# Kernel optimization log

Hardware: AMD Instinct MI355X
Metric: run time of the kernel (lower is better)

The kernel has to match this reference:

```python
import jax, jax.numpy as jnp
import numpy as np

D_MODEL = 1024
NUM_HEADS = 16

def setup_inputs() -> dict:
    key = jax.random.key(0)
    ks = jax.random.split(key, 5)
    std = np.sqrt(2.0 / (D_MODEL + D_MODEL))
    def w(k):
        # trunc_normal approx: normal clipped to +-3 std
        v = jax.random.truncated_normal(k, -3.0, 3.0, (D_MODEL, D_MODEL), dtype=jnp.float32) * std
        return v
    return {
        "x": jax.random.normal(ks[0], (2, 2048, D_MODEL), dtype=jnp.float32),
        "w_q": w(ks[1]),
        "w_k": w(ks[2]),
        "w_v": w(ks[3]),
        "w_o": w(ks[4]),
    }

def reference(x, w_q, w_k, w_v, w_o):
    B, S, D = x.shape
    H = NUM_HEADS
    dk = D // H
    # Linear: y = x @ W^T  (weight is [d_out, d_in])
    def proj(w):
        y = jnp.einsum('bsd,ed->bse', x, w)
        return y.reshape(B, S, H, dk).transpose(0, 2, 1, 3)  # [B,H,S,dk]
    q, k, v = proj(w_q), proj(w_k), proj(w_v)
    scale = 1.0 / jnp.sqrt(jnp.float32(dk))
    scores = jnp.einsum('bhqd,bhkd->bhqk', q, k) * scale  # [B,H,S,S]
    causal = jnp.tril(jnp.ones((S, S), dtype=bool))
    scores = jnp.where(causal, scores, -jnp.inf)
    attn = jax.nn.softmax(scores, axis=-1)
    out = jnp.einsum('bhqk,bhkd->bhqd', attn, v)  # [B,H,S,dk]
    out = out.transpose(0, 2, 1, 3).reshape(B, S, D)
    return jnp.einsum('bsd,ed->bse', out, w_o)
```

## Files before the change

### kernel.cpp

```cpp
#include <hip/hip_runtime.h>
#include <hip/hip_bf16.h>
#include <stdint.h>

#define S_LEN 2048
#define DM    1024
#define NH    16
#define DK    64
#define NBATCH 2

typedef __attribute__((ext_vector_type(8))) short bf8_t;
typedef __attribute__((ext_vector_type(4))) short s4_t;
typedef __attribute__((ext_vector_type(4))) float f4_t;

using bf16 = __hip_bfloat16;

#define NEG_BIG (-1.0e30f)
#define SCALE2  (0.125f * 1.44269504088896f)

static __device__ __forceinline__ f4_t mfma16(bf8_t a, bf8_t b, f4_t c) {
    return __builtin_amdgcn_mfma_f32_16x16x32_bf16(a, b, c, 0, 0, 0);
}

static __device__ __forceinline__ short f2b(float f) {
    __hip_bfloat16 h = __float2bfloat16(f);
    return *reinterpret_cast<short*>(&h);
}

static __device__ __forceinline__ void g2l16(const bf16* g, bf16* l) {
#if __has_builtin(__builtin_amdgcn_global_load_lds)
    __builtin_amdgcn_global_load_lds(
        (const __attribute__((address_space(1))) void*)g,
        (__attribute__((address_space(3))) void*)l, 16, 0, 0);
#else
    *(bf8_t*)l = *(const bf8_t*)g;
#endif
}

__global__ __launch_bounds__(256)
void cvt_all(const float* __restrict__ x,  const float* __restrict__ wq,
             const float* __restrict__ wk, const float* __restrict__ wv,
             const float* __restrict__ wo, bf16* __restrict__ ob) {
    const size_t SEG = 1u << 20;
    size_t i = ((size_t)blockIdx.x * 256 + threadIdx.x) * 8;
    const float* src;
    if      (i < 4 * SEG) src = x  + i;
    else if (i < 5 * SEG) src = wq + (i - 4 * SEG);
    else if (i < 6 * SEG) src = wk + (i - 5 * SEG);
    else if (i < 7 * SEG) src = wv + (i - 6 * SEG);
    else                  src = wo + (i - 7 * SEG);
    float4 f0 = *(const float4*)(src);
    float4 f1 = *(const float4*)(src + 4);
    bf8_t v;
    v[0]=f2b(f0.x); v[1]=f2b(f0.y); v[2]=f2b(f0.z); v[3]=f2b(f0.w);
    v[4]=f2b(f1.x); v[5]=f2b(f1.y); v[6]=f2b(f1.z); v[7]=f2b(f1.w);
    *(bf8_t*)(ob + i) = v;
}

#define GEMM_B_MAINLOOP(Aptr, Bptr)                                          \
    __shared__ bf16 As[128][32];                                             \
    __shared__ bf16 Bs[128][32];                                             \
    const int tid  = threadIdx.x;                                            \
    const int lane = tid & 63;                                               \
    const int w    = tid >> 6;                                               \
    const int wr   = w >> 1, wc = w & 1;                                     \
    const int lhi  = lane >> 4, llo = lane & 15;                             \
    const int bm   = blockIdx.x * 128;                                       \
    const int bn   = blockIdx.y * 128;                                       \
    const int r0c  = tid >> 2;                           \
    const int c0c  = (tid & 3) << 3;                     \
    const int r1c  = (256 + tid) >> 2;                                       \
    f4_t acc[4][4] = {};                                                     \
    for (int k0 = 0; k0 < 1024; k0 += 32) {                                  \
        __syncthreads();                                                     \
        g2l16(Aptr + (size_t)(bm + r0c) * 1024 + k0 + c0c,                   \
              &As[0][0] + (size_t)tid * 8);                                  \
        g2l16(Aptr + (size_t)(bm + r1c) * 1024 + k0 + c0c,                   \
              &As[0][0] + (size_t)(256 + tid) * 8);                          \
        g2l16(Bptr + (size_t)(bn + r0c) * 1024 + k0 + c0c,                   \
              &Bs[0][0] + (size_t)tid * 8);                                  \
        g2l16(Bptr + (size_t)(bn + r1c) * 1024 + k0 + c0c,                   \
              &Bs[0][0] + (size_t)(256 + tid) * 8);                          \
        asm volatile("s_waitcnt vmcnt(0)" ::: "memory");                     \
        __syncthreads();                                                     \
        bf8_t af[4], bfr[4];                                                 \
        _Pragma("unroll")                                                    \
        for (int i = 0; i < 4; ++i) {                                        \
            af[i]  = *(const bf8_t*)(&As[wr * 64 + i * 16 + llo][lhi * 8]);  \
            bfr[i] = *(const bf8_t*)(&Bs[wc * 64 + i * 16 + llo][lhi * 8]);  \
        }                                                                    \
        _Pragma("unroll")                                                    \
        for (int mi = 0; mi < 4; ++mi)                                       \
            _Pragma("unroll")                                                \
            for (int ni = 0; ni < 4; ++ni)                                   \
                acc[mi][ni] = mfma16(af[mi], bfr[ni], acc[mi][ni]);          \
    }

__global__ __launch_bounds__(256)
void gemm_qkv_b(const bf16* __restrict__ xb,
                const bf16* __restrict__ wqb, const bf16* __restrict__ wkb,
                const bf16* __restrict__ wvb,
                bf16* __restrict__ qws, bf16* __restrict__ kws,
                bf16* __restrict__ vtws) {
    const int z = blockIdx.z;
    const bf16* Wb = (z == 0) ? wqb : (z == 1) ? wkb : wvb;
    GEMM_B_MAINLOOP(xb, Wb)

    if (z < 2) {
        bf16* C = z ? kws : qws;
        const float sc = z ? 1.0f : SCALE2;
        #pragma unroll
        for (int mi = 0; mi < 4; ++mi)
            #pragma unroll
            for (int ni = 0; ni < 4; ++ni)
                #pragma unroll
                for (int r = 0; r < 4; ++r) {
                    int m = bm + wr * 64 + mi * 16 + lhi * 4 + r;
                    int n = bn + wc * 64 + ni * 16 + llo;
                    int b = m >> 11, s = m & (S_LEN - 1);
                    int h = n >> 6,  d = n & (DK - 1);
                    C[(((size_t)(b * NH + h) * S_LEN) + s) * DK + d] =
                        __float2bfloat16(acc[mi][ni][r] * sc);
                }
    } else {
        #pragma unroll
        for (int mi = 0; mi < 4; ++mi)
            #pragma unroll
            for (int ni = 0; ni < 4; ++ni) {
                int m0 = bm + wr * 64 + mi * 16 + lhi * 4;
                int n  = bn + wc * 64 + ni * 16 + llo;
                int b = m0 >> 11, s0 = m0 & (S_LEN - 1);
                int h = n >> 6,   d  = n & (DK - 1);
                s4_t pk;
                #pragma unroll
                for (int r = 0; r < 4; ++r) pk[r] = f2b(acc[mi][ni][r]);
                *(s4_t*)&vtws[(((size_t)(b * NH + h) * DK) + d) * S_LEN + s0] = pk;
            }
    }
}

__global__ __launch_bounds__(256)
void gemm_o_b(const bf16* __restrict__ A, const bf16* __restrict__ Wb,
              float* __restrict__ C) {
    __shared__ bf16 As[128][32];
    __shared__ bf16 Bs[64][32];
    const int tid  = threadIdx.x;
    const int lane = tid & 63;
    const int w    = tid >> 6;
    const int wr   = w >> 1, wc = w & 1;
    const int lhi  = lane >> 4, llo = lane & 15;
    const int bm   = blockIdx.x * 128;
    const int bn   = blockIdx.y * 64;
    const int r0c  = tid >> 2;
    const int c0c  = (tid & 3) << 3;
    const int r1c  = (256 + tid) >> 2;
    f4_t acc[4][2] = {};
    for (int k0 = 0; k0 < 1024; k0 += 32) {
        __syncthreads();
        g2l16(A + (size_t)(bm + r0c) * 1024 + k0 + c0c,
              &As[0][0] + (size_t)tid * 8);
        g2l16(A + (size_t)(bm + r1c) * 1024 + k0 + c0c,
              &As[0][0] + (size_t)(256 + tid) * 8);
        g2l16(Wb + (size_t)(bn + r0c) * 1024 + k0 + c0c,
              &Bs[0][0] + (size_t)tid * 8);
        asm volatile("s_waitcnt vmcnt(0)" ::: "memory");
        __syncthreads();
        bf8_t af[4], bfr[2];
        #pragma unroll
        for (int i = 0; i < 4; ++i)
            af[i] = *(const bf8_t*)(&As[wr * 64 + i * 16 + llo][lhi * 8]);
        #pragma unroll
        for (int i = 0; i < 2; ++i)
            bfr[i] = *(const bf8_t*)(&Bs[wc * 32 + i * 16 + llo][lhi * 8]);
        #pragma unroll
        for (int mi = 0; mi < 4; ++mi)
            #pragma unroll
            for (int ni = 0; ni < 2; ++ni)
                acc[mi][ni] = mfma16(af[mi], bfr[ni], acc[mi][ni]);
    }
    #pragma unroll
    for (int mi = 0; mi < 4; ++mi)
        #pragma unroll
        for (int ni = 0; ni < 2; ++ni)
            #pragma unroll
            for (int r = 0; r < 4; ++r) {
                int m = bm + wr * 64 + mi * 16 + lhi * 4 + r;
                int n = bn + wc * 32 + ni * 16 + llo;
                C[(size_t)m * DM + n] = acc[mi][ni][r];
            }
}

__global__ __launch_bounds__(256)
void gemm_qkv_f32(const float* __restrict__ x,
                  const float* __restrict__ wqp, const float* __restrict__ wkp,
                  const float* __restrict__ wvp,
                  bf16* __restrict__ qws, bf16* __restrict__ kws,
                  bf16* __restrict__ vtws) {
    constexpr int K = DM;
    constexpr int BM = 128, BK = 32, LDT = BK + 8;
    const int z = blockIdx.z;
    const float* W = (z == 0) ? wqp : (z == 1) ? wkp : wvp;
    __shared__ bf16 As[BM][LDT];
    __shared__ bf16 Bs[BM][LDT];
    const int tid  = threadIdx.x;
    const int lane = tid & 63;
    const int w    = tid >> 6;
    const int wr   = w >> 1, wc = w & 1;
    const int lhi  = lane >> 4, llo = lane & 15;
    const int bm   = blockIdx.x * BM;
    const int bn   = blockIdx.y * BM;
    f4_t acc[4][4] = {};
    for (int k0 = 0; k0 < K; k0 += BK) {
        __syncthreads();
        #pragma unroll
        for (int t = 0; t < 2; ++t) {
            int c   = t * 256 + tid;
            int row = c >> 2;
            int col = (c & 3) << 3;
            {
                const float* s0 = x + (size_t)(bm + row) * K + k0 + col;
                float4 f0 = *(const float4*)(s0);
                float4 f1 = *(const float4*)(s0 + 4);
                bf8_t a8;
                a8[0]=f2b(f0.x); a8[1]=f2b(f0.y); a8[2]=f2b(f0.z); a8[3]=f2b(f0.w);
                a8[4]=f2b(f1.x); a8[5]=f2b(f1.y); a8[6]=f2b(f1.z); a8[7]=f2b(f1.w);
                *(bf8_t*)(&As[row][col]) = a8;
            }
            {
                const float* s0 = W + (size_t)(bn + row) * K + k0 + col;
                float4 f0 = *(const float4*)(s0);
                float4 f1 = *(const float4*)(s0 + 4);
                bf8_t b8;
                b8[0]=f2b(f0.x); b8[1]=f2b(f0.y); b8[2]=f2b(f0.z); b8[3]=f2b(f0.w);
                b8[4]=f2b(f1.x); b8[5]=f2b(f1.y); b8[6]=f2b(f1.z); b8[7]=f2b(f1.w);
                *(bf8_t*)(&Bs[row][col]) = b8;
            }
        }
        __syncthreads();
        bf8_t af[4], bfr[4];
        #pragma unroll
        for (int i = 0; i < 4; ++i) {
            af[i]  = *(const bf8_t*)(&As[wr * 64 + i * 16 + llo][lhi * 8]);
            bfr[i] = *(const bf8_t*)(&Bs[wc * 64 + i * 16 + llo][lhi * 8]);
        }
        #pragma unroll
        for (int mi = 0; mi < 4; ++mi)
            #pragma unroll
            for (int ni = 0; ni < 4; ++ni)
                acc[mi][ni] = mfma16(af[mi], bfr[ni], acc[mi][ni]);
    }
    if (z < 2) {
        bf16* C = z ? kws : qws;
        const float sc = z ? 1.0f : SCALE2;
        #pragma unroll
        for (int mi = 0; mi < 4; ++mi)
            #pragma unroll
            for (int ni = 0; ni < 4; ++ni)
                #pragma unroll
                for (int r = 0; r < 4; ++r) {
                    int m = bm + wr * 64 + mi * 16 + lhi * 4 + r;
                    int n = bn + wc * 64 + ni * 16 + llo;
                    int b = m >> 11, s = m & (S_LEN - 1);
                    int h = n >> 6,  d = n & (DK - 1);
                    C[(((size_t)(b * NH + h) * S_LEN) + s) * DK + d] =
                        __float2bfloat16(acc[mi][ni][r] * sc);
                }
    } else {
        #pragma unroll
        for (int mi = 0; mi < 4; ++mi)
            #pragma unroll
            for (int ni = 0; ni < 4; ++ni) {
                int m0 = bm + wr * 64 + mi * 16 + lhi * 4;
                int n  = bn + wc * 64 + ni * 16 + llo;
                int b = m0 >> 11, s0 = m0 & (S_LEN - 1);
                int h = n >> 6,   d  = n & (DK - 1);
                s4_t pk;
                #pragma unroll
                for (int r = 0; r < 4; ++r) pk[r] = f2b(acc[mi][ni][r]);
                *(s4_t*)&vtws[(((size_t)(b * NH + h) * DK) + d) * S_LEN + s0] = pk;
            }
    }
}

__global__ __launch_bounds__(256)
void gemm_o_f32(const bf16* __restrict__ A, const float* __restrict__ W,
                float* __restrict__ C) {
    constexpr int N = DM;
    constexpr int K = DM;
    constexpr int BM = 128, BN = 64, BK = 32, LDT = BK + 8;
    __shared__ bf16 As[BM][LDT];
    __shared__ bf16 Bs[BN][LDT];
    const int tid  = threadIdx.x;
    const int lane = tid & 63;
    const int w    = tid >> 6;
    const int wr   = w >> 1, wc = w & 1;
    const int lhi  = lane >> 4, llo = lane & 15;
    const int bm   = blockIdx.x * BM;
    const int bn   = blockIdx.y * BN;
    f4_t acc[4][2] = {};
    for (int k0 = 0; k0 < K; k0 += BK) {
        __syncthreads();
        #pragma unroll
        for (int t = 0; t < 2; ++t) {
            int c   = t * 256 + tid;
            int row = c >> 2;
            int col = (c & 3) << 3;
            *(bf8_t*)(&As[row][col]) =
                *(const bf8_t*)(A + (size_t)(bm + row) * K + k0 + col);
        }
        {
            int row = tid >> 2;
            int col = (tid & 3) << 3;
            const float* s0 = W + (size_t)(bn + row) * K + k0 + col;
            float4 f0 = *(const float4*)(s0);
            float4 f1 = *(const float4*)(s0 + 4);
            bf8_t b8;
            b8[0]=f2b(f0.x); b8[1]=f2b(f0.y); b8[2]=f2b(f0.z); b8[3]=f2b(f0.w);
            b8[4]=f2b(f1.x); b8[5]=f2b(f1.y); b8[6]=f2b(f1.z); b8[7]=f2b(f1.w);
            *(bf8_t*)(&Bs[row][col]) = b8;
        }
        __syncthreads();
        bf8_t af[4], bfr[2];
        #pragma unroll
        for (int i = 0; i < 4; ++i)
            af[i] = *(const bf8_t*)(&As[wr * 64 + i * 16 + llo][lhi * 8]);
        #pragma unroll
        for (int i = 0; i < 2; ++i)
            bfr[i] = *(const bf8_t*)(&Bs[wc * 32 + i * 16 + llo][lhi * 8]);
        #pragma unroll
        for (int mi = 0; mi < 4; ++mi)
            #pragma unroll
            for (int ni = 0; ni < 2; ++ni)
                acc[mi][ni] = mfma16(af[mi], bfr[ni], acc[mi][ni]);
    }
    #pragma unroll
    for (int mi = 0; mi < 4; ++mi)
        #pragma unroll
        for (int ni = 0; ni < 2; ++ni)
            #pragma unroll
            for (int r = 0; r < 4; ++r) {
                int m = bm + wr * 64 + mi * 16 + lhi * 4 + r;
                int n = bn + wc * 32 + ni * 16 + llo;
                C[(size_t)m * N + n] = acc[mi][ni][r];
            }
}

__global__ __launch_bounds__(512, 4)
void attn_fwd(const bf16* __restrict__ Q, const bf16* __restrict__ K,
              const bf16* __restrict__ Vt, bf16* __restrict__ AO) {
    __shared__ bf16 Ks[2][64][64];
    __shared__ bf16 Vs[2][64][64];

    const int bh = blockIdx.x;
    const int qt = 15 - (int)blockIdx.y;
    const int q0 = qt * 128;
    const int nt = 2 * qt + 2;

    const bf16* Qh = Q  + (size_t)bh * S_LEN * DK;
    const bf16* Kh = K  + (size_t)bh * S_LEN * DK;
    const bf16* Vh = Vt + (size_t)bh * DK * S_LEN;

    const int tid  = threadIdx.x;
    const int lane = tid & 63;
    const int w    = tid >> 6;
    const int lhi  = lane >> 4, llo = lane & 15;
    const int qw   = q0 + w * 16;
    const int sw   = llo & 7;

    const int srow = tid >> 3;
    const int schk = (tid & 7) ^ (srow & 7);
    const int gk = (((srow >> 2) & 3) << 3) | (((srow >> 4) & 1) << 2)
                 | (srow & 3) | ((srow >> 5) << 5);

#define STAGE(kv, b)                                                          \
    do {                                                                      \
        g2l16(Kh + (size_t)((kv) + gk) * DK + schk * 8,                       \
              &Ks[b][0][0] + (size_t)tid * 8);                                \
        g2l16(Vh + (size_t)srow * S_LEN + (kv) + schk * 8,                    \
              &Vs[b][0][0] + (size_t)tid * 8);                                \
    } while (0)

    const bf16* qrow = Qh + (size_t)(q0 + w * 16 + llo) * DK;
    const bf8_t qf0 = *(const bf8_t*)(qrow + lhi * 8);
    const bf8_t qf1 = *(const bf8_t*)(qrow + 32 + lhi * 8);

    bf8_t ones;
    #pragma unroll
    for (int j = 0; j < 8; ++j) ones[j] = (short)0x3F80;

    STAGE(0, 0);
    asm volatile("s_waitcnt vmcnt(0)" ::: "memory");
    __syncthreads();

    f4_t o[4] = {};
    float lr[4] = {0.f, 0.f, 0.f, 0.f};
    float mr = NEG_BIG;

    for (int t = 0; t < nt; ++t) {
        const int kv0 = t * 64;
        const int cur = t & 1;

        if (t + 1 < nt) STAGE((t + 1) * 64, cur ^ 1);

        if (kv0 <= qw + 15) {
            f4_t s[4] = {};
            __builtin_amdgcn_s_setprio(1);
            #pragma unroll
            for (int nf = 0; nf < 4; ++nf) {
                const int R = nf * 16 + llo;
                bf8_t k0f = *(const bf8_t*)&Ks[cur][R][(lhi ^ sw) * 8];
                bf8_t k1f = *(const bf8_t*)&Ks[cur][R][((4 + lhi) ^ sw) * 8];
                s[nf] = mfma16(k0f, qf0, s[nf]);
                s[nf] = mfma16(k1f, qf1, s[nf]);
            }
            __builtin_amdgcn_s_setprio(0);

            if (kv0 + 63 > qw) {
                #pragma unroll
                for (int nf = 0; nf < 4; ++nf)
                    #pragma unroll
                    for (int r = 0; r < 4; ++r)
                        if (kv0 + lhi * 8 + ((nf & 1) << 2) + r + ((nf >> 1) << 5)
                            > qw + llo)
                            s[nf][r] = NEG_BIG;
            }

            float pm = s[0][0];
            #pragma unroll
            for (int nf = 0; nf < 4; ++nf)
                #pragma unroll
                for (int r = 0; r < 4; ++r) pm = fmaxf(pm, s[nf][r]);
            pm = fmaxf(pm, __shfl_xor(pm, 16));
            pm = fmaxf(pm, __shfl_xor(pm, 32));

            if (__any(pm > mr + 8.0f)) {
                float mn = fmaxf(mr, pm);
                float alpha = exp2f(mr - mn);
                mr = mn;
                float ao[4];
                #pragma unroll
                for (int r = 0; r < 4; ++r) ao[r] = __shfl(alpha, lhi * 4 + r);
                #pragma unroll
                for (int df = 0; df < 4; ++df)
                    #pragma unroll
                    for (int r = 0; r < 4; ++r) o[df][r] *= ao[r];
                #pragma unroll
                for (int r = 0; r < 4; ++r) lr[r] *= ao[r];
            }

            bf8_t pa0, pa1;
            #pragma unroll
            for (int r = 0; r < 4; ++r) {
                pa0[r]     = f2b(exp2f(s[0][r] - mr));
                pa0[4 + r] = f2b(exp2f(s[1][r] - mr));
                pa1[r]     = f2b(exp2f(s[2][r] - mr));
                pa1[4 + r] = f2b(exp2f(s[3][r] - mr));
            }

            f4_t rsacc = {};
            rsacc = mfma16(pa0, ones, rsacc);
            rsacc = mfma16(pa1, ones, rsacc);

            __builtin_amdgcn_s_setprio(1);
            #pragma unroll
            for (int df = 0; df < 4; ++df) {
                const int R = df * 16 + llo;
                bf8_t vb0 = *(const bf8_t*)&Vs[cur][R][(lhi ^ sw) * 8];
                bf8_t vb1 = *(const bf8_t*)&Vs[cur][R][((4 + lhi) ^ sw) * 8];
                o[df] = mfma16(pa0, vb0, o[df]);
                o[df] = mfma16(pa1, vb1, o[df]);
            }
            __builtin_amdgcn_s_setprio(0);

            #pragma unroll
            for (int r = 0; r < 4; ++r) lr[r] += rsacc[r];
        }

        asm volatile("s_waitcnt vmcnt(0)" ::: "memory");
        __syncthreads();
    }
#undef STAGE

    const int b = bh >> 4, h = bh & (NH - 1);
    #pragma unroll
    for (int r = 0; r < 4; ++r) {
        float inv = 1.0f / lr[r];
        int q = q0 + w * 16 + lhi * 4 + r;
        bf16* orow = AO + ((size_t)(b * S_LEN + q) * DM) + h * DK;
        #pragma unroll
        for (int df = 0; df < 4; ++df)
            orow[df * 16 + llo] = __float2bfloat16(o[df][r] * inv);
    }
}

extern "C" void kernel_launch(void* const* d_in, const int* in_sizes, int n_in,
                              void* d_out, int out_size, void* d_ws, size_t ws_size,
                              hipStream_t stream) {
    const float* x  = (const float*)d_in[0];
    const float* wq = (const float*)d_in[1];
    const float* wk = (const float*)d_in[2];
    const float* wv = (const float*)d_in[3];
    const float* wo = (const float*)d_in[4];
    float* out = (float*)d_out;

    const size_t SEG   = 1u << 20;
    const size_t elems = 4 * SEG;
    const size_t need_fast = (8 * SEG + 3 * elems) * sizeof(bf16);

    dim3 blk(256);

    if (ws_size >= need_fast) {
        bf16* ob   = (bf16*)d_ws;
        bf16* xb   = ob;
        bf16* wqb  = ob + 4 * SEG;
        bf16* wkb  = ob + 5 * SEG;
        bf16* wvb  = ob + 6 * SEG;
        bf16* wob  = ob + 7 * SEG;
        bf16* qws  = ob + 8 * SEG;
        bf16* kws  = qws + elems;
        bf16* vtws = kws + elems;
        bf16* aws  = xb;

        cvt_all<<<4096, blk, 0, stream>>>(x, wq, wk, wv, wo, ob);
        gemm_qkv_b<<<dim3(32, 8, 3), blk, 0, stream>>>(xb, wqb, wkb, wvb,
                                                       qws, kws, vtws);
        attn_fwd<<<dim3(NBATCH * NH, 16), dim3(512), 0, stream>>>(qws, kws, vtws, aws);
        gemm_o_b<<<dim3(32, 16), blk, 0, stream>>>(aws, wob, out);
    } else {
        if (ws_size < elems * 4 * sizeof(bf16)) return;
        bf16* qws  = (bf16*)d_ws;
        bf16* kws  = qws + elems;
        bf16* vtws = kws + elems;
        bf16* aws  = vtws + elems;

        gemm_qkv_f32<<<dim3(32, 8, 3), blk, 0, stream>>>(x, wq, wk, wv,
                                                         qws, kws, vtws);
        attn_fwd<<<dim3(NBATCH * NH, 16), dim3(512), 0, stream>>>(qws, kws, vtws, aws);
        gemm_o_f32<<<dim3(32, 16), blk, 0, stream>>>(aws, wo, out);
    }
}
```

Baseline: 113.4 us.

## Process two 16-row query tiles per wave in attention with 256-thread blocks

The attention kernel drops from 512 to 256 threads per block, and each wave now handles two 16-row query tiles (A and B) instead of one. Each K and V fragment read from LDS feeds twice as many MFMAs, and each thread stages twice as many global-to-LDS chunks. This roughly halves LDS read traffic per unit of work and the number of waves sharing a barrier. The cost is higher register pressure (launch bounds now 256,2) and less parallelism per block to hide latency. Causal skipping for the lower tile is handled per tile with a doA flag.

```diff
diff --git a/kernel.cpp b/kernel.cpp
--- a/kernel.cpp
+++ b/kernel.cpp
@@ -344,7 +344,7 @@
             }
 }
 
-__global__ __launch_bounds__(512, 4)
+__global__ __launch_bounds__(256, 2)
 void attn_fwd(const bf16* __restrict__ Q, const bf16* __restrict__ K,
               const bf16* __restrict__ Vt, bf16* __restrict__ AO) {
     __shared__ bf16 Ks[2][64][64];
@@ -363,25 +363,32 @@
     const int lane = tid & 63;
     const int w    = tid >> 6;
     const int lhi  = lane >> 4, llo = lane & 15;
-    const int qw   = q0 + w * 16;
+    const int qwA  = q0 + w * 32;
+    const int qwB  = qwA + 16;
     const int sw   = llo & 7;
 
-    const int srow = tid >> 3;
-    const int schk = (tid & 7) ^ (srow & 7);
-    const int gk = (((srow >> 2) & 3) << 3) | (((srow >> 4) & 1) << 2)
-                 | (srow & 3) | ((srow >> 5) << 5);
+    const int r0   = tid >> 3;
+    const int schk = (tid & 7) ^ (r0 & 7);
+    const int gk0  = (((r0 >> 2) & 3) << 3) | (((r0 >> 4) & 1) << 2) | (r0 & 3);
 
 #define STAGE(kv, b)                                                          \
     do {                                                                      \
-        g2l16(Kh + (size_t)((kv) + gk) * DK + schk * 8,                       \
+        g2l16(Kh + (size_t)((kv) + gk0) * DK + schk * 8,                      \
               &Ks[b][0][0] + (size_t)tid * 8);                                \
-        g2l16(Vh + (size_t)srow * S_LEN + (kv) + schk * 8,                    \
+        g2l16(Kh + (size_t)((kv) + gk0 + 32) * DK + schk * 8,                 \
+              &Ks[b][32][0] + (size_t)tid * 8);                               \
+        g2l16(Vh + (size_t)r0 * S_LEN + (kv) + schk * 8,                      \
               &Vs[b][0][0] + (size_t)tid * 8);                                \
+        g2l16(Vh + (size_t)(r0 + 32) * S_LEN + (kv) + schk * 8,               \
+              &Vs[b][32][0] + (size_t)tid * 8);                               \
     } while (0)
 
-    const bf16* qrow = Qh + (size_t)(q0 + w * 16 + llo) * DK;
-    const bf8_t qf0 = *(const bf8_t*)(qrow + lhi * 8);
-    const bf8_t qf1 = *(const bf8_t*)(qrow + 32 + lhi * 8);
+    const bf16* qrowA = Qh + (size_t)(qwA + llo) * DK;
+    const bf16* qrowB = Qh + (size_t)(qwB + llo) * DK;
+    const bf8_t qfA0 = *(const bf8_t*)(qrowA + lhi * 8);
+    const bf8_t qfA1 = *(const bf8_t*)(qrowA + 32 + lhi * 8);
+    const bf8_t qfB0 = *(const bf8_t*)(qrowB + lhi * 8);
+    const bf8_t qfB1 = *(const bf8_t*)(qrowB + 32 + lhi * 8);
 
     bf8_t ones;
     #pragma unroll
@@ -391,9 +398,9 @@
     asm volatile("s_waitcnt vmcnt(0)" ::: "memory");
     __syncthreads();
 
-    f4_t o[4] = {};
-    float lr[4] = {0.f, 0.f, 0.f, 0.f};
-    float mr = NEG_BIG;
+    f4_t oA[4] = {}, oB[4] = {};
+    float lrA[4] = {0.f,0.f,0.f,0.f}, lrB[4] = {0.f,0.f,0.f,0.f};
+    float mrA = NEG_BIG, mrB = NEG_BIG;
 
     for (int t = 0; t < nt; ++t) {
         const int kv0 = t * 64;
@@ -401,64 +408,108 @@
 
         if (t + 1 < nt) STAGE((t + 1) * 64, cur ^ 1);
 
-        if (kv0 <= qw + 15) {
-            f4_t s[4] = {};
+        if (kv0 <= qwB + 15) {
+            const bool doA = (kv0 <= qwA + 15);
+
+            f4_t sA[4] = {}, sB[4] = {};
             __builtin_amdgcn_s_setprio(1);
             #pragma unroll
             for (int nf = 0; nf < 4; ++nf) {
                 const int R = nf * 16 + llo;
                 bf8_t k0f = *(const bf8_t*)&Ks[cur][R][(lhi ^ sw) * 8];
                 bf8_t k1f = *(const bf8_t*)&Ks[cur][R][((4 + lhi) ^ sw) * 8];
-                s[nf] = mfma16(k0f, qf0, s[nf]);
-                s[nf] = mfma16(k1f, qf1, s[nf]);
+                sB[nf] = mfma16(k0f, qfB0, sB[nf]);
+                sB[nf] = mfma16(k1f, qfB1, sB[nf]);
+                if (doA) {
+                    sA[nf] = mfma16(k0f, qfA0, sA[nf]);
+                    sA[nf] = mfma16(k1f, qfA1, sA[nf]);
+                }
             }
             __builtin_amdgcn_s_setprio(0);
 
-            if (kv0 + 63 > qw) {
+            if (kv0 + 63 > qwB) {
                 #pragma unroll
                 for (int nf = 0; nf < 4; ++nf)
                     #pragma unroll
                     for (int r = 0; r < 4; ++r)
                         if (kv0 + lhi * 8 + ((nf & 1) << 2) + r + ((nf >> 1) << 5)
-                            > qw + llo)
-                            s[nf][r] = NEG_BIG;
-            }
-
-            float pm = s[0][0];
+                            > qwB + llo)
+                            sB[nf][r] = NEG_BIG;
+            }
+            if (doA && kv0 + 63 > qwA) {
+                #pragma unroll
+                for (int nf = 0; nf < 4; ++nf)
+                    #pragma unroll
+                    for (int r = 0; r < 4; ++r)
+                        if (kv0 + lhi * 8 + ((nf & 1) << 2) + r + ((nf >> 1) << 5)
+                            > qwA + llo)
+                            sA[nf][r] = NEG_BIG;
+            }
+
+            float pmA = NEG_BIG, pmB = sB[0][0];
             #pragma unroll
             for (int nf = 0; nf < 4; ++nf)
                 #pragma unroll
-                for (int r = 0; r < 4; ++r) pm = fmaxf(pm, s[nf][r]);
-            pm = fmaxf(pm, __shfl_xor(pm, 16));
-            pm = fmaxf(pm, __shfl_xor(pm, 32));
-
-            if (__any(pm > mr + 8.0f)) {
-                float mn = fmaxf(mr, pm);
-                float alpha = exp2f(mr - mn);
-                mr = mn;
-                float ao[4];
-                #pragma unroll
-                for (int r = 0; r < 4; ++r) ao[r] = __shfl(alpha, lhi * 4 + r);
+                for (int r = 0; r < 4; ++r) pmB = fmaxf(pmB, sB[nf][r]);
+            if (doA) {
+                pmA = sA[0][0];
+                #pragma unroll
+                for (int nf = 0; nf < 4; ++nf)
+                    #pragma unroll
+                    for (int r = 0; r < 4; ++r) pmA = fmaxf(pmA, sA[nf][r]);
+            }
+            pmB = fmaxf(pmB, __shfl_xor(pmB, 16));
+            pmB = fmaxf(pmB, __shfl_xor(pmB, 32));
+            pmA = fmaxf(pmA, __shfl_xor(pmA, 16));
+            pmA = fmaxf(pmA, __shfl_xor(pmA, 32));
+
+            if (__any(fmaxf(pmA - mrA, pmB - mrB) > 8.0f)) {
+                float mnA = fmaxf(mrA, pmA), mnB = fmaxf(mrB, pmB);
+                float aA = exp2f(mrA - mnA), aB = exp2f(mrB - mnB);
+                mrA = mnA; mrB = mnB;
+                float aoA[4], aoB[4];
+                #pragma unroll
+                for (int r = 0; r < 4; ++r) {
+                    aoA[r] = __shfl(aA, lhi * 4 + r);
+                    aoB[r] = __shfl(aB, lhi * 4 + r);
+                }
                 #pragma unroll
                 for (int df = 0; df < 4; ++df)
                     #pragma unroll
-                    for (int r = 0; r < 4; ++r) o[df][r] *= ao[r];
-                #pragma unroll
-                for (int r = 0; r < 4; ++r) lr[r] *= ao[r];
-            }
-
-            bf8_t pa0, pa1;
+                    for (int r = 0; r < 4; ++r) {
+                        oA[df][r] *= aoA[r];
+                        oB[df][r] *= aoB[r];
+                    }
+                #pragma unroll
+                for (int r = 0; r < 4; ++r) { lrA[r] *= aoA[r]; lrB[r] *= aoB[r]; }
+            }
+
+            bf8_t paA0 = ones, paA1 = ones, paB0, paB1;
             #pragma unroll
             for (int r = 0; r < 4; ++r) {
-                pa0[r]     = f2b(exp2f(s[0][r] - mr));
-                pa0[4 + r] = f2b(exp2f(s[1][r] - mr));
-                pa1[r]     = f2b(exp2f(s[2][r] - mr));
-                pa1[4 + r] = f2b(exp2f(s[3][r] - mr));
-            }
-
-            f4_t rsacc = {};
-            rsacc = mfma16(pa0, ones, rsacc);
-            rsacc = mfma16(pa1, ones, rsacc);
+                paB0[r]     = f2b(exp2f(sB[0][r] - mrB));
+                paB0[4 + r] = f2b(exp2f(sB[1][r] - mrB));
+                paB1[r]     = f2b(exp2f(sB[2][r] - mrB));
+                paB1[4 + r] = f2b(exp2f(sB[3][r] - mrB));
+            }
+            if (doA) {
+                #pragma unroll
+                for (int r = 0; r < 4; ++r) {
+                    paA0[r]     = f2b(exp2f(sA[0][r] - mrA));
+                    paA0[4 + r] = f2b(exp2f(sA[1][r] - mrA));
+                    paA1[r]     = f2b(exp2f(sA[2][r] - mrA));
+                    paA1[4 + r] = f2b(exp2f(sA[3][r] - mrA));
+                }
+            }
+
+            f4_t rsB = {};
+            rsB = mfma16(paB0, ones, rsB);
+            rsB = mfma16(paB1, ones, rsB);
+            f4_t rsA = {};
+            if (doA) {
+                rsA = mfma16(paA0, ones, rsA);
+                rsA = mfma16(paA1, ones, rsA);
+            }
 
             __builtin_amdgcn_s_setprio(1);
             #pragma unroll
@@ -466,13 +517,20 @@
                 const int R = df * 16 + llo;
                 bf8_t vb0 = *(const bf8_t*)&Vs[cur][R][(lhi ^ sw) * 8];
                 bf8_t vb1 = *(const bf8_t*)&Vs[cur][R][((4 + lhi) ^ sw) * 8];
-                o[df] = mfma16(pa0, vb0, o[df]);
-                o[df] = mfma16(pa1, vb1, o[df]);
+                oB[df] = mfma16(paB0, vb0, oB[df]);
+                oB[df] = mfma16(paB1, vb1, oB[df]);
+                if (doA) {
+                    oA[df] = mfma16(paA0, vb0, oA[df]);
+                    oA[df] = mfma16(paA1, vb1, oA[df]);
+                }
             }
             __builtin_amdgcn_s_setprio(0);
 
             #pragma unroll
-            for (int r = 0; r < 4; ++r) lr[r] += rsacc[r];
+            for (int r = 0; r < 4; ++r) {
+                lrB[r] += rsB[r];
+                if (doA) lrA[r] += rsA[r];
+            }
         }
 
         asm volatile("s_waitcnt vmcnt(0)" ::: "memory");
@@ -483,12 +541,17 @@
     const int b = bh >> 4, h = bh & (NH - 1);
     #pragma unroll
     for (int r = 0; r < 4; ++r) {
-        float inv = 1.0f / lr[r];
-        int q = q0 + w * 16 + lhi * 4 + r;
-        bf16* orow = AO + ((size_t)(b * S_LEN + q) * DM) + h * DK;
-        #pragma unroll
-        for (int df = 0; df < 4; ++df)
-            orow[df * 16 + llo] = __float2bfloat16(o[df][r] * inv);
+        float invA = 1.0f / lrA[r];
+        float invB = 1.0f / lrB[r];
+        int qA = qwA + lhi * 4 + r;
+        int qB = qwB + lhi * 4 + r;
+        bf16* orowA = AO + ((size_t)(b * S_LEN + qA) * DM) + h * DK;
+        bf16* orowB = AO + ((size_t)(b * S_LEN + qB) * DM) + h * DK;
+        #pragma unroll
+        for (int df = 0; df < 4; ++df) {
+            orowA[df * 16 + llo] = __float2bfloat16(oA[df][r] * invA);
+            orowB[df * 16 + llo] = __float2bfloat16(oB[df][r] * invB);
+        }
     }
 }
 
@@ -523,7 +586,7 @@
         cvt_all<<<4096, blk, 0, stream>>>(x, wq, wk, wv, wo, ob);
         gemm_qkv_b<<<dim3(32, 8, 3), blk, 0, stream>>>(xb, wqb, wkb, wvb,
                                                        qws, kws, vtws);
-        attn_fwd<<<dim3(NBATCH * NH, 16), dim3(512), 0, stream>>>(qws, kws, vtws, aws);
+        attn_fwd<<<dim3(NBATCH * NH, 16), blk, 0, stream>>>(qws, kws, vtws, aws);
         gemm_o_b<<<dim3(32, 16), blk, 0, stream>>>(aws, wob, out);
     } else {
         if (ws_size < elems * 4 * sizeof(bf16)) return;
@@ -534,7 +597,7 @@
 
         gemm_qkv_f32<<<dim3(32, 8, 3), blk, 0, stream>>>(x, wq, wk, wv,
                                                          qws, kws, vtws);
-        attn_fwd<<<dim3(NBATCH * NH, 16), dim3(512), 0, stream>>>(qws, kws, vtws, aws);
+        attn_fwd<<<dim3(NBATCH * NH, 16), blk, 0, stream>>>(qws, kws, vtws, aws);
         gemm_o_f32<<<dim3(32, 16), blk, 0, stream>>>(aws, wo, out);
     }
 }
```

After: 130.9 us. 15.4% more time.

## Split KV range across two warp groups per 64-row query tile with merge

Applied to the files above, without the earlier changes.

The attention kernel now processes 64 query rows per block instead of 128, and splits the KV tiles between two groups of four waves that work on alternating tiles at the same time. Each group keeps its own double-buffered K/V shared-memory tiles. At the end the partial outputs, row sums and maxima are exchanged through shared memory and merged flash-decoding style. This doubles the grid and halves the serial KV loop per wave to improve parallelism and load balance, at the cost of more redundant K/V loads, twice the shared memory, and a final merge step.

```diff
diff --git a/kernel.cpp b/kernel.cpp
--- a/kernel.cpp
+++ b/kernel.cpp
@@ -347,13 +347,14 @@
 __global__ __launch_bounds__(512, 4)
 void attn_fwd(const bf16* __restrict__ Q, const bf16* __restrict__ K,
               const bf16* __restrict__ Vt, bf16* __restrict__ AO) {
-    __shared__ bf16 Ks[2][64][64];
-    __shared__ bf16 Vs[2][64][64];
+    __shared__ bf16 Ks[2][2][64][64];
+    __shared__ bf16 Vs[2][2][64][64];
 
     const int bh = blockIdx.x;
-    const int qt = 15 - (int)blockIdx.y;
-    const int q0 = qt * 128;
-    const int nt = 2 * qt + 2;
+    const int qt = 31 - (int)blockIdx.y;
+    const int q0 = qt * 64;
+    const int nt = qt + 1;
+    const int S  = (nt + 1) >> 1;
 
     const bf16* Qh = Q  + (size_t)bh * S_LEN * DK;
     const bf16* Kh = K  + (size_t)bh * S_LEN * DK;
@@ -362,8 +363,10 @@
     const int tid  = threadIdx.x;
     const int lane = tid & 63;
     const int w    = tid >> 6;
+    const int g    = w >> 2;
+    const int qsub = w & 3;
     const int lhi  = lane >> 4, llo = lane & 15;
-    const int qw   = q0 + w * 16;
+    const int qw   = q0 + qsub * 16;
     const int sw   = llo & 7;
 
     const int srow = tid >> 3;
@@ -371,15 +374,16 @@
     const int gk = (((srow >> 2) & 3) << 3) | (((srow >> 4) & 1) << 2)
                  | (srow & 3) | ((srow >> 5) << 5);
 
-#define STAGE(kv, b)                                                          \
+#define STAGE(t, gg, b)                                                       \
     do {                                                                      \
-        g2l16(Kh + (size_t)((kv) + gk) * DK + schk * 8,                       \
-              &Ks[b][0][0] + (size_t)tid * 8);                                \
-        g2l16(Vh + (size_t)srow * S_LEN + (kv) + schk * 8,                    \
-              &Vs[b][0][0] + (size_t)tid * 8);                                \
+        const int kv_ = (t) * 64;                                             \
+        g2l16(Kh + (size_t)(kv_ + gk) * DK + schk * 8,                        \
+              &Ks[gg][b][0][0] + (size_t)tid * 8);                            \
+        g2l16(Vh + (size_t)srow * S_LEN + kv_ + schk * 8,                     \
+              &Vs[gg][b][0][0] + (size_t)tid * 8);                            \
     } while (0)
 
-    const bf16* qrow = Qh + (size_t)(q0 + w * 16 + llo) * DK;
+    const bf16* qrow = Qh + (size_t)(qw + llo) * DK;
     const bf8_t qf0 = *(const bf8_t*)(qrow + lhi * 8);
     const bf8_t qf1 = *(const bf8_t*)(qrow + 32 + lhi * 8);
 
@@ -387,7 +391,8 @@
     #pragma unroll
     for (int j = 0; j < 8; ++j) ones[j] = (short)0x3F80;
 
-    STAGE(0, 0);
+    STAGE(0, 0, 0);
+    if (1 < nt) STAGE(1, 1, 0);
     asm volatile("s_waitcnt vmcnt(0)" ::: "memory");
     __syncthreads();
 
@@ -395,22 +400,24 @@
     float lr[4] = {0.f, 0.f, 0.f, 0.f};
     float mr = NEG_BIG;
 
-    for (int t = 0; t < nt; ++t) {
-        const int kv0 = t * 64;
-        const int cur = t & 1;
-
-        if (t + 1 < nt) STAGE((t + 1) * 64, cur ^ 1);
-
-        if (kv0 <= qw + 15) {
-            f4_t s[4] = {};
+    for (int s = 0; s < S; ++s) {
+        const int tg  = 2 * s + g;
+        const int cur = s & 1;
+        const int tn0 = 2 * (s + 1);
+        if (tn0 < nt)     STAGE(tn0,     0, cur ^ 1);
+        if (tn0 + 1 < nt) STAGE(tn0 + 1, 1, cur ^ 1);
+
+        const int kv0 = tg * 64;
+        if (tg < nt && kv0 <= qw + 15) {
+            f4_t sc[4] = {};
             __builtin_amdgcn_s_setprio(1);
             #pragma unroll
             for (int nf = 0; nf < 4; ++nf) {
                 const int R = nf * 16 + llo;
-                bf8_t k0f = *(const bf8_t*)&Ks[cur][R][(lhi ^ sw) * 8];
-                bf8_t k1f = *(const bf8_t*)&Ks[cur][R][((4 + lhi) ^ sw) * 8];
-                s[nf] = mfma16(k0f, qf0, s[nf]);
-                s[nf] = mfma16(k1f, qf1, s[nf]);
+                bf8_t k0f = *(const bf8_t*)&Ks[g][cur][R][(lhi ^ sw) * 8];
+                bf8_t k1f = *(const bf8_t*)&Ks[g][cur][R][((4 + lhi) ^ sw) * 8];
+                sc[nf] = mfma16(k0f, qf0, sc[nf]);
+                sc[nf] = mfma16(k1f, qf1, sc[nf]);
             }
             __builtin_amdgcn_s_setprio(0);
 
@@ -421,14 +428,14 @@
                     for (int r = 0; r < 4; ++r)
                         if (kv0 + lhi * 8 + ((nf & 1) << 2) + r + ((nf >> 1) << 5)
                             > qw + llo)
-                            s[nf][r] = NEG_BIG;
-            }
-
-            float pm = s[0][0];
+                            sc[nf][r] = NEG_BIG;
+            }
+
+            float pm = sc[0][0];
             #pragma unroll
             for (int nf = 0; nf < 4; ++nf)
                 #pragma unroll
-                for (int r = 0; r < 4; ++r) pm = fmaxf(pm, s[nf][r]);
+                for (int r = 0; r < 4; ++r) pm = fmaxf(pm, sc[nf][r]);
             pm = fmaxf(pm, __shfl_xor(pm, 16));
             pm = fmaxf(pm, __shfl_xor(pm, 32));
 
@@ -450,10 +457,10 @@
             bf8_t pa0, pa1;
             #pragma unroll
             for (int r = 0; r < 4; ++r) {
-                pa0[r]     = f2b(exp2f(s[0][r] - mr));
-                pa0[4 + r] = f2b(exp2f(s[1][r] - mr));
-                pa1[r]     = f2b(exp2f(s[2][r] - mr));
-                pa1[4 + r] = f2b(exp2f(s[3][r] - mr));
+                pa0[r]     = f2b(exp2f(sc[0][r] - mr));
+                pa0[4 + r] = f2b(exp2f(sc[1][r] - mr));
+                pa1[r]     = f2b(exp2f(sc[2][r] - mr));
+                pa1[4 + r] = f2b(exp2f(sc[3][r] - mr));
             }
 
             f4_t rsacc = {};
@@ -464,8 +471,8 @@
             #pragma unroll
             for (int df = 0; df < 4; ++df) {
                 const int R = df * 16 + llo;
-                bf8_t vb0 = *(const bf8_t*)&Vs[cur][R][(lhi ^ sw) * 8];
-                bf8_t vb1 = *(const bf8_t*)&Vs[cur][R][((4 + lhi) ^ sw) * 8];
+                bf8_t vb0 = *(const bf8_t*)&Vs[g][cur][R][(lhi ^ sw) * 8];
+                bf8_t vb1 = *(const bf8_t*)&Vs[g][cur][R][((4 + lhi) ^ sw) * 8];
                 o[df] = mfma16(pa0, vb0, o[df]);
                 o[df] = mfma16(pa1, vb1, o[df]);
             }
@@ -480,15 +487,40 @@
     }
 #undef STAGE
 
-    const int b = bh >> 4, h = bh & (NH - 1);
+    float mo[4];
     #pragma unroll
-    for (int r = 0; r < 4; ++r) {
-        float inv = 1.0f / lr[r];
-        int q = q0 + w * 16 + lhi * 4 + r;
-        bf16* orow = AO + ((size_t)(b * S_LEN + q) * DM) + h * DK;
+    for (int r = 0; r < 4; ++r) mo[r] = __shfl(mr, lhi * 4 + r);
+
+    float* xch = (float*)&Ks[0][0][0][0];
+    if (g == 1) {
+        float* p = xch + ((size_t)(qsub * 64 + lane)) * 24;
         #pragma unroll
         for (int df = 0; df < 4; ++df)
-            orow[df * 16 + llo] = __float2bfloat16(o[df][r] * inv);
+            #pragma unroll
+            for (int r = 0; r < 4; ++r) p[df * 4 + r] = o[df][r];
+        #pragma unroll
+        for (int r = 0; r < 4; ++r) { p[16 + r] = lr[r]; p[20 + r] = mo[r]; }
+    }
+    __syncthreads();
+    if (g == 0) {
+        const float* p = xch + ((size_t)(qsub * 64 + lane)) * 24;
+        const int b = bh >> 4, h = bh & (NH - 1);
+        #pragma unroll
+        for (int r = 0; r < 4; ++r) {
+            float m1 = p[20 + r];
+            float M  = fmaxf(mo[r], m1);
+            float a0 = exp2f(mo[r] - M);
+            float a1 = exp2f(m1 - M);
+            float l  = lr[r] * a0 + p[16 + r] * a1;
+            float inv = 1.0f / l;
+            int q = qw + lhi * 4 + r;
+            bf16* orow = AO + ((size_t)(b * S_LEN + q) * DM) + h * DK;
+            #pragma unroll
+            for (int df = 0; df < 4; ++df) {
+                float v = o[df][r] * a0 + p[df * 4 + r] * a1;
+                orow[df * 16 + llo] = __float2bfloat16(v * inv);
+            }
+        }
     }
 }
 
@@ -523,7 +555,7 @@
         cvt_all<<<4096, blk, 0, stream>>>(x, wq, wk, wv, wo, ob);
         gemm_qkv_b<<<dim3(32, 8, 3), blk, 0, stream>>>(xb, wqb, wkb, wvb,
                                                        qws, kws, vtws);
-        attn_fwd<<<dim3(NBATCH * NH, 16), dim3(512), 0, stream>>>(qws, kws, vtws, aws);
+        attn_fwd<<<dim3(NBATCH * NH, 32), dim3(512), 0, stream>>>(qws, kws, vtws, aws);
         gemm_o_b<<<dim3(32, 16), blk, 0, stream>>>(aws, wob, out);
     } else {
         if (ws_size < elems * 4 * sizeof(bf16)) return;
@@ -534,7 +566,7 @@
 
         gemm_qkv_f32<<<dim3(32, 8, 3), blk, 0, stream>>>(x, wq, wk, wv,
                                                          qws, kws, vtws);
-        attn_fwd<<<dim3(NBATCH * NH, 16), dim3(512), 0, stream>>>(qws, kws, vtws, aws);
+        attn_fwd<<<dim3(NBATCH * NH, 32), dim3(512), 0, stream>>>(qws, kws, vtws, aws);
         gemm_o_f32<<<dim3(32, 16), blk, 0, stream>>>(aws, wo, out);
     }
 }
```

Result: faster. 103.6 us, median of 2 (-8.6%).
